# Kernel tuning notes

Hardware: AMD Instinct MI355X
Metric: run time of the kernel (lower is better)

Reference implementation:

```python
import jax, jax.numpy as jnp
import numpy as np

B, S, E, NUM_CLASSES = 4, 4096, 256, 16

def setup_inputs() -> dict:
    key = jax.random.key(0)
    ks = jax.random.split(key, 10)
    std = E ** -0.5
    return {
        "x":  jax.random.normal(ks[0], (B, S, E), dtype=jnp.float32),
        "wq": jax.random.normal(ks[1], (E, E), dtype=jnp.float32) * std,
        "bq": jnp.zeros((E,), dtype=jnp.float32),
        "wk": jax.random.normal(ks[2], (E, E), dtype=jnp.float32) * std,
        "bk": jnp.zeros((E,), dtype=jnp.float32),
        "wv": jax.random.normal(ks[3], (E, E), dtype=jnp.float32) * std,
        "bv": jnp.zeros((E,), dtype=jnp.float32),
        "wo": jax.random.normal(ks[4], (NUM_CLASSES, E), dtype=jnp.float32) * std,
        "bo": jnp.zeros((NUM_CLASSES,), dtype=jnp.float32),
    }

def reference(x, wq, bq, wk, bk, wv, bv, wo, bo):
    embed_dim = wq.shape[0]
    scaling = embed_dim ** -0.5  # float(embed_dim) ** (-0.5)
    # torch Linear: y = x @ W.T + b
    Q = jnp.einsum('bse,oe->bso', x, wq) + bq
    K = jnp.einsum('bse,oe->bso', x, wk) + bk
    V = jnp.einsum('bse,oe->bso', x, wv) + bv
    # scores: [B, S, S]
    scores = jnp.einsum('bqe,bke->bqk', Q, K) * scaling
    # original code has `/ (embed_dim ^ 0.5)`; intended math is / sqrt(embed_dim)
    attn = jax.nn.softmax(scores, axis=-1) * scaling
    attn_out = jnp.einsum('bqk,bke->bqe', attn, V)
    return jnp.einsum('bqe,oe->bqo', attn_out, wo) + bo
```

## Files before the change

kernel.cpp:

```cpp
#include <hip/hip_runtime.h>
#include <hip/hip_bf16.h>


#define S_ 4096
#define E_ 256
#define B_ 4
#define NC_ 16
#define BS_ (B_ * S_)
#define NS_ 4

typedef __attribute__((ext_vector_type(8))) short bf16x8;
typedef __attribute__((ext_vector_type(4))) float f32x4;

__device__ __forceinline__ unsigned short bf16_rtne(float f) {
    unsigned int u = __float_as_uint(f);
    return (unsigned short)((u + 0x7FFFu + ((u >> 16) & 1u)) >> 16);
}
__device__ __forceinline__ bf16x8 pack8(f32x4 a, f32x4 b) {
    bf16x8 r;
#pragma unroll
    for (int i = 0; i < 4; i++) r[i] = (short)bf16_rtne(a[i]);
#pragma unroll
    for (int i = 0; i < 4; i++) r[4 + i] = (short)bf16_rtne(b[i]);
    return r;
}
__device__ __forceinline__ void gl_lds16(const void* g, void* lds) {
    __builtin_amdgcn_global_load_lds(
        (const __attribute__((address_space(1))) unsigned int*)g,
        (__attribute__((address_space(3))) unsigned int*)lds, 16, 0, 0);
}

__global__ __launch_bounds__(256) void qkv_gemm(
    const float* __restrict__ x, const float* __restrict__ wq,
    const float* __restrict__ wk, const float* __restrict__ wv,
    const float* __restrict__ bq, const float* __restrict__ bk,
    const float* __restrict__ bv, short* __restrict__ Qb,
    short* __restrict__ Kb, short* __restrict__ Vtc) {
    __shared__ bf16x8 xt2[512];
    __shared__ bf16x8 wt2[2048];
    __shared__ short epi[16896];

    int t = threadIdx.x;
    int sel = blockIdx.x, m0 = blockIdx.y * 64;
    int lane = t & 63, wid = t >> 6, quad = lane >> 4, idx = lane & 15;

    const float* w = (sel == 0) ? wq : (sel == 1) ? wk : wv;
    const float* bias = (sel == 0) ? bq : (sel == 1) ? bk : bv;

    const float* xsrc = x + (size_t)(m0 + (t >> 2)) * E_ + (t & 3) * 8;

    f32x4 zf = {0.f, 0.f, 0.f, 0.f};
    f32x4 acc[16];
#pragma unroll
    for (int i = 0; i < 16; i++) acc[i] = zf;

    f32x4 xa0 = *(const f32x4*)xsrc;
    f32x4 xa1 = *(const f32x4*)(xsrc + 4);
    f32x4 wa[4][2];
#pragma unroll
    for (int i = 0; i < 4; i++) {
        int p = i * 256 + t;
        const float* ws = w + (size_t)(p >> 2) * E_ + (p & 3) * 8;
        wa[i][0] = *(const f32x4*)ws;
        wa[i][1] = *(const f32x4*)(ws + 4);
    }

    for (int kci = 0; kci < 8; kci++) {
        int par = kci & 1;
        xt2[par * 256 + t] = pack8(xa0, xa1);
#pragma unroll
        for (int i = 0; i < 4; i++) wt2[par * 1024 + i * 256 + t] = pack8(wa[i][0], wa[i][1]);
        if (kci < 7) {
            int kc = (kci + 1) * 32;
            xa0 = *(const f32x4*)(xsrc + kc);
            xa1 = *(const f32x4*)(xsrc + kc + 4);
#pragma unroll
            for (int i = 0; i < 4; i++) {
                int p = i * 256 + t;
                const float* ws = w + (size_t)(p >> 2) * E_ + (p & 3) * 8 + kc;
                wa[i][0] = *(const f32x4*)ws;
                wa[i][1] = *(const f32x4*)(ws + 4);
            }
        }
        __syncthreads();
        bf16x8 af = xt2[par * 256 + (wid * 16 + idx) * 4 + quad];
#pragma unroll
        for (int ct = 0; ct < 16; ct++)
            acc[ct] = __builtin_amdgcn_mfma_f32_16x16x32_bf16(
                af, wt2[par * 1024 + (ct * 16 + idx) * 4 + quad], acc[ct], 0, 0, 0);
    }
    __syncthreads();

    int qr = quad * 4;
    if (sel == 2) {
#pragma unroll
        for (int ct = 0; ct < 16; ct++) {
            int e = ct * 16 + idx;
            float bb = bias[e];
#pragma unroll
            for (int r = 0; r < 4; r++) {
                int mr = wid * 16 + qr + r;
                int ckg = mr >> 5, sin = mr & 31;
                int sp = ((sin & 15) << 1) | (sin >> 4);
                int pos = (sp >> 3) ^ ((e >> 1) & 3);
                epi[ckg * 8192 + e * 32 + pos * 8 + (sp & 7)] =
                    (short)bf16_rtne(acc[ct][r] + bb);
            }
        }
        __syncthreads();
        size_t base = ((size_t)((m0 >> 12) * 128 + ((m0 & (S_ - 1)) >> 5))) * 8192;
#pragma unroll
        for (int j = 0; j < 8; j++) {
            int unit = j * 256 + t;
            *(bf16x8*)(Vtc + base + (size_t)unit * 8) = *(const bf16x8*)&epi[unit * 8];
        }
    } else {
        float alpha = (sel == 0) ? 0.0625f : 1.0f;
#pragma unroll
        for (int ct = 0; ct < 16; ct++) {
            int n = ct * 16 + idx;
            float bb = bias[n];
#pragma unroll
            for (int r = 0; r < 4; r++) {
                int row = wid * 16 + qr + r;
                int col = (sel == 1) ? ((((n >> 3) ^ (row & 7)) << 3) | (n & 7)) : n;
                epi[row * 264 + col] = (short)bf16_rtne((acc[ct][r] + bb) * alpha);
            }
        }
        __syncthreads();
        short* out = (sel == 0) ? Qb : Kb;
#pragma unroll
        for (int j = 0; j < 8; j++) {
            int g = j * 256 + t;
            int row = g >> 5, seg = g & 31;
            *(bf16x8*)(out + (size_t)(m0 + row) * E_ + seg * 8) =
                *(const bf16x8*)&epi[row * 264 + seg * 8];
        }
    }
}

__global__ __launch_bounds__(256, 2) void flash_attn(
    const short* __restrict__ Qb, const short* __restrict__ Kb,
    const short* __restrict__ Vtc, short* __restrict__ Opart,
    float* __restrict__ lpart) {
    __shared__ __align__(16) short lds[36864];

    int t = threadIdx.x;
    int b = blockIdx.z, slice = blockIdx.y, q0 = blockIdx.x * 128;
    int key0 = slice * (S_ / NS_);
    const int nchunk = (S_ / NS_) / 32;
    int lane = t & 63, wv = t >> 6, quad = lane >> 4, idx = lane & 15;

    bf16x8 qf[2][8];
#pragma unroll
    for (int u = 0; u < 2; u++) {
        const short* qrow = Qb + (size_t)(b * S_ + q0 + u * 64 + wv * 16 + idx) * E_ + quad * 8;
#pragma unroll
        for (int c = 0; c < 8; c++) qf[u][c] = *(const bf16x8*)(qrow + c * 32);
    }

    f32x4 zf = {0.f, 0.f, 0.f, 0.f};
    f32x4 oacc[2][16];
#pragma unroll
    for (int u = 0; u < 2; u++)
#pragma unroll
        for (int i = 0; i < 16; i++) oacc[u][i] = zf;
    float ls[2][4] = {{0, 0, 0, 0}, {0, 0, 0, 0}};

    const short* kg = Kb + (size_t)(b * S_ + key0) * E_ + lane * 8;
    const short* vg = Vtc + ((size_t)(b * 128 + (key0 >> 5))) * 8192 + lane * 8;
    short* psw = lds + 32768 + wv * 1024;
    unsigned int* pswu = (unsigned int*)psw;
    int vsw = (quad ^ ((idx >> 1) & 3)) << 3;

#pragma unroll
    for (int j = 0; j < 4; j++) gl_lds16(kg + (wv * 4 + j) * 512, &lds[(wv * 4 + j) * 512]);
#pragma unroll
    for (int j = 0; j < 4; j++) gl_lds16(vg + (wv * 4 + j) * 512, &lds[16384 + (wv * 4 + j) * 512]);
#pragma unroll
    for (int j = 0; j < 4; j++) gl_lds16(kg + 8192 + (wv * 4 + j) * 512, &lds[8192 + (wv * 4 + j) * 512]);
    __syncthreads();

    {
        f32x4 s[4] = {zf, zf, zf, zf};
#pragma unroll
        for (int c = 0; c < 8; c++) {
            int p = (((c * 4 + quad) ^ (idx & 7)) << 3);
            bf16x8 k0 = *(const bf16x8*)&lds[idx * 256 + p];
            bf16x8 k1 = *(const bf16x8*)&lds[(16 + idx) * 256 + p];
            s[0] = __builtin_amdgcn_mfma_f32_16x16x32_bf16(qf[0][c], k0, s[0], 0, 0, 0);
            s[1] = __builtin_amdgcn_mfma_f32_16x16x32_bf16(qf[0][c], k1, s[1], 0, 0, 0);
            s[2] = __builtin_amdgcn_mfma_f32_16x16x32_bf16(qf[1][c], k0, s[2], 0, 0, 0);
            s[3] = __builtin_amdgcn_mfma_f32_16x16x32_bf16(qf[1][c], k1, s[3], 0, 0, 0);
        }
#pragma unroll
        for (int r = 0; r < 4; r++) {
            float a0 = __expf(s[0][r]), a1 = __expf(s[1][r]);
            float c0 = __expf(s[2][r]), c1 = __expf(s[3][r]);
            ls[0][r] += a0 + a1;
            ls[1][r] += c0 + c1;
            pswu[(quad * 4 + r) * 16 + idx] =
                (unsigned int)bf16_rtne(a0) | ((unsigned int)bf16_rtne(a1) << 16);
            pswu[256 + (quad * 4 + r) * 16 + idx] =
                (unsigned int)bf16_rtne(c0) | ((unsigned int)bf16_rtne(c1) << 16);
        }
    }

    for (int ck = 0; ck < nchunk - 1; ck++) {
        __syncthreads();
        if (ck + 2 < nchunk) {
            const short* ks = kg + (size_t)(ck + 2) * 8192;
            short* kd = lds + (ck & 1) * 8192;
#pragma unroll
            for (int j = 0; j < 4; j++) gl_lds16(ks + (wv * 4 + j) * 512, &kd[(wv * 4 + j) * 512]);
        }
        {
            const short* vs = vg + (size_t)(ck + 1) * 8192;
            short* vd = lds + 16384 + ((ck + 1) & 1) * 8192;
#pragma unroll
            for (int j = 0; j < 4; j++) gl_lds16(vs + (wv * 4 + j) * 512, &vd[(wv * 4 + j) * 512]);
        }
        const short* kc = lds + ((ck + 1) & 1) * 8192;
        f32x4 s[4] = {zf, zf, zf, zf};
#pragma unroll
        for (int c = 0; c < 8; c++) {
            int p = (((c * 4 + quad) ^ (idx & 7)) << 3);
            bf16x8 k0 = *(const bf16x8*)&kc[idx * 256 + p];
            bf16x8 k1 = *(const bf16x8*)&kc[(16 + idx) * 256 + p];
            s[0] = __builtin_amdgcn_mfma_f32_16x16x32_bf16(qf[0][c], k0, s[0], 0, 0, 0);
            s[1] = __builtin_amdgcn_mfma_f32_16x16x32_bf16(qf[0][c], k1, s[1], 0, 0, 0);
            s[2] = __builtin_amdgcn_mfma_f32_16x16x32_bf16(qf[1][c], k0, s[2], 0, 0, 0);
            s[3] = __builtin_amdgcn_mfma_f32_16x16x32_bf16(qf[1][c], k1, s[3], 0, 0, 0);
        }
        bf16x8 af0 = *(const bf16x8*)&psw[idx * 32 + quad * 8];
        bf16x8 af1 = *(const bf16x8*)&psw[512 + idx * 32 + quad * 8];
#pragma unroll
        for (int r = 0; r < 4; r++) {
            float a0 = __expf(s[0][r]), a1 = __expf(s[1][r]);
            float c0 = __expf(s[2][r]), c1 = __expf(s[3][r]);
            ls[0][r] += a0 + a1;
            ls[1][r] += c0 + c1;
            pswu[(quad * 4 + r) * 16 + idx] =
                (unsigned int)bf16_rtne(a0) | ((unsigned int)bf16_rtne(a1) << 16);
            pswu[256 + (quad * 4 + r) * 16 + idx] =
                (unsigned int)bf16_rtne(c0) | ((unsigned int)bf16_rtne(c1) << 16);
        }
        const short* vc = lds + 16384 + (ck & 1) * 8192;
#pragma unroll
        for (int ct = 0; ct < 16; ct++) {
            bf16x8 v = *(const bf16x8*)&vc[(ct * 16 + idx) * 32 + vsw];
            oacc[0][ct] = __builtin_amdgcn_mfma_f32_16x16x32_bf16(af0, v, oacc[0][ct], 0, 0, 0);
            oacc[1][ct] = __builtin_amdgcn_mfma_f32_16x16x32_bf16(af1, v, oacc[1][ct], 0, 0, 0);
        }
    }
    __syncthreads();
    {
        bf16x8 af0 = *(const bf16x8*)&psw[idx * 32 + quad * 8];
        bf16x8 af1 = *(const bf16x8*)&psw[512 + idx * 32 + quad * 8];
        const short* vc = lds + 16384 + ((nchunk - 1) & 1) * 8192;
#pragma unroll
        for (int ct = 0; ct < 16; ct++) {
            bf16x8 v = *(const bf16x8*)&vc[(ct * 16 + idx) * 32 + vsw];
            oacc[0][ct] = __builtin_amdgcn_mfma_f32_16x16x32_bf16(af0, v, oacc[0][ct], 0, 0, 0);
            oacc[1][ct] = __builtin_amdgcn_mfma_f32_16x16x32_bf16(af1, v, oacc[1][ct], 0, 0, 0);
        }
    }
    __syncthreads();

#pragma unroll
    for (int u = 0; u < 2; u++)
#pragma unroll
        for (int r = 0; r < 4; r++) {
            float v = ls[u][r];
            v += __shfl_xor(v, 1);
            v += __shfl_xor(v, 2);
            v += __shfl_xor(v, 4);
            v += __shfl_xor(v, 8);
            if (idx == 0)
                lpart[(size_t)slice * BS_ + b * S_ + q0 + u * 64 + wv * 16 + quad * 4 + r] = v;
        }

    short* scr = lds + wv * 8192;
#pragma unroll
    for (int u = 0; u < 2; u++)
#pragma unroll
        for (int ct = 0; ct < 16; ct++) {
            int e = ct * 16 + idx;
#pragma unroll
            for (int r = 0; r < 4; r++) {
                int lr = quad * 4 + r;
                scr[u * 4096 + lr * 256 + ((((e >> 3) ^ (lr & 7)) << 3) | (e & 7))] =
                    (short)bf16_rtne(oacc[u][ct][r]);
            }
        }
#pragma unroll
    for (int u = 0; u < 2; u++) {
        size_t obase = ((size_t)slice * BS_ + (size_t)b * S_ + q0 + u * 64 + wv * 16) * E_;
#pragma unroll
        for (int j = 0; j < 8; j++) {
            int unit = j * 64 + lane;
            *(bf16x8*)(Opart + obase + (size_t)unit * 8) =
                *(const bf16x8*)&scr[u * 4096 + unit * 8];
        }
    }
}

__global__ __launch_bounds__(256) void proj_out(
    const short* __restrict__ Opart, const float* __restrict__ lpart,
    const float* __restrict__ wo, const float* __restrict__ bo,
    float* __restrict__ out) {
    __shared__ __align__(16) short at2[2][16384];
    int t = threadIdx.x;
    int m0 = blockIdx.x * 64;
    int lane = t & 63, wv = t >> 6, quad = lane >> 4, idx = lane & 15;

    bf16x8 bw[8];
#pragma unroll
    for (int c = 0; c < 8; c++) {
        const float* ws = wo + idx * E_ + c * 32 + quad * 8;
        f32x4 w0 = *(const f32x4*)ws;
        f32x4 w1 = *(const f32x4*)(ws + 4);
        bw[c] = pack8(w0, w1);
    }

#pragma unroll
    for (int j = 0; j < 8; j++)
        gl_lds16(Opart + (size_t)m0 * E_ + (wv * 8 + j) * 512 + lane * 8,
                 &at2[0][(wv * 8 + j) * 512]);

    f32x4 acc = {0.f, 0.f, 0.f, 0.f};
    for (int ns = 0; ns < NS_; ns++) {
        __syncthreads();
        if (ns + 1 < NS_) {
            const short* src = Opart + ((size_t)(ns + 1) * BS_ + m0) * E_ + lane * 8;
#pragma unroll
            for (int j = 0; j < 8; j++)
                gl_lds16(src + (wv * 8 + j) * 512, &at2[(ns + 1) & 1][(wv * 8 + j) * 512]);
        }
        const short* a = at2[ns & 1];
#pragma unroll
        for (int c = 0; c < 8; c++) {
            bf16x8 af = *(const bf16x8*)&a[(wv * 16 + idx) * 256 +
                                           ((((c * 4 + quad) ^ (idx & 7)) << 3))];
            acc = __builtin_amdgcn_mfma_f32_16x16x32_bf16(af, bw[c], acc, 0, 0, 0);
        }
    }
#pragma unroll
    for (int r = 0; r < 4; r++) {
        int m = m0 + wv * 16 + quad * 4 + r;
        float ltot = 0.f;
#pragma unroll
        for (int ns = 0; ns < NS_; ns++) ltot += lpart[(size_t)ns * BS_ + m];
        out[(size_t)m * NC_ + idx] = acc[r] * (0.0625f / ltot) + bo[idx];
    }
}

extern "C" void kernel_launch(void* const* d_in, const int* in_sizes, int n_in,
                              void* d_out, int out_size, void* d_ws, size_t ws_size,
                              hipStream_t stream) {
    const float* x  = (const float*)d_in[0];
    const float* wq = (const float*)d_in[1];
    const float* bq = (const float*)d_in[2];
    const float* wk = (const float*)d_in[3];
    const float* bk = (const float*)d_in[4];
    const float* wv = (const float*)d_in[5];
    const float* bv = (const float*)d_in[6];
    const float* wo = (const float*)d_in[7];
    const float* bo = (const float*)d_in[8];
    float* out = (float*)d_out;

    const size_t NEL = (size_t)BS_ * E_;
    short* Qb = (short*)d_ws;
    short* Kb = Qb + NEL;
    short* Vtc = Kb + NEL;
    short* Opart = Vtc + NEL;
    float* lpart = (float*)(Opart + (size_t)NS_ * NEL);

    qkv_gemm<<<dim3(3, BS_ / 64), 256, 0, stream>>>(x, wq, wk, wv, bq, bk, bv, Qb, Kb, Vtc);
    flash_attn<<<dim3(S_ / 128, NS_, B_), 256, 0, stream>>>(Qb, Kb, Vtc, Opart, lpart);
    proj_out<<<BS_ / 64, 256, 0, stream>>>(Opart, lpart, wo, bo, out);
}
```

Baseline: 182.5 us.

## Fuse output projection into flash attention epilogue with atomic split-K reduction

```diff
diff --git a/kernel.cpp b/kernel.cpp
--- a/kernel.cpp
+++ b/kernel.cpp
@@ -141,8 +141,8 @@
 
 __global__ __launch_bounds__(256, 2) void flash_attn(
     const short* __restrict__ Qb, const short* __restrict__ Kb,
-    const short* __restrict__ Vtc, short* __restrict__ Opart,
-    float* __restrict__ lpart) {
+    const short* __restrict__ Vtc, const float* __restrict__ wo,
+    float* __restrict__ acc, float* __restrict__ ltot) {
     __shared__ __align__(16) short lds[36864];
 
     int t = threadIdx.x;
@@ -157,6 +157,14 @@
         const short* qrow = Qb + (size_t)(b * S_ + q0 + u * 64 + wv * 16 + idx) * E_ + quad * 8;
 #pragma unroll
         for (int c = 0; c < 8; c++) qf[u][c] = *(const bf16x8*)(qrow + c * 32);
+    }
+    bf16x8 bw[8];
+#pragma unroll
+    for (int c = 0; c < 8; c++) {
+        const float* ws = wo + idx * E_ + c * 32 + quad * 8;
+        f32x4 w0 = *(const f32x4*)ws;
+        f32x4 w1 = *(const f32x4*)(ws + 4);
+        bw[c] = pack8(w0, w1);
     }
 
     f32x4 zf = {0.f, 0.f, 0.f, 0.f};
@@ -277,7 +285,7 @@
             v += __shfl_xor(v, 4);
             v += __shfl_xor(v, 8);
             if (idx == 0)
-                lpart[(size_t)slice * BS_ + b * S_ + q0 + u * 64 + wv * 16 + quad * 4 + r] = v;
+                atomicAdd(&ltot[(size_t)b * S_ + q0 + u * 64 + wv * 16 + quad * 4 + r], v);
         }
 
     short* scr = lds + wv * 8192;
@@ -293,66 +301,34 @@
                     (short)bf16_rtne(oacc[u][ct][r]);
             }
         }
-#pragma unroll
-    for (int u = 0; u < 2; u++) {
-        size_t obase = ((size_t)slice * BS_ + (size_t)b * S_ + q0 + u * 64 + wv * 16) * E_;
-#pragma unroll
-        for (int j = 0; j < 8; j++) {
-            int unit = j * 64 + lane;
-            *(bf16x8*)(Opart + obase + (size_t)unit * 8) =
-                *(const bf16x8*)&scr[u * 4096 + unit * 8];
-        }
-    }
-}
-
-__global__ __launch_bounds__(256) void proj_out(
-    const short* __restrict__ Opart, const float* __restrict__ lpart,
-    const float* __restrict__ wo, const float* __restrict__ bo,
-    float* __restrict__ out) {
-    __shared__ __align__(16) short at2[2][16384];
-    int t = threadIdx.x;
-    int m0 = blockIdx.x * 64;
-    int lane = t & 63, wv = t >> 6, quad = lane >> 4, idx = lane & 15;
-
-    bf16x8 bw[8];
-#pragma unroll
-    for (int c = 0; c < 8; c++) {
-        const float* ws = wo + idx * E_ + c * 32 + quad * 8;
-        f32x4 w0 = *(const f32x4*)ws;
-        f32x4 w1 = *(const f32x4*)(ws + 4);
-        bw[c] = pack8(w0, w1);
-    }
-
-#pragma unroll
-    for (int j = 0; j < 8; j++)
-        gl_lds16(Opart + (size_t)m0 * E_ + (wv * 8 + j) * 512 + lane * 8,
-                 &at2[0][(wv * 8 + j) * 512]);
-
-    f32x4 acc = {0.f, 0.f, 0.f, 0.f};
-    for (int ns = 0; ns < NS_; ns++) {
-        __syncthreads();
-        if (ns + 1 < NS_) {
-            const short* src = Opart + ((size_t)(ns + 1) * BS_ + m0) * E_ + lane * 8;
-#pragma unroll
-            for (int j = 0; j < 8; j++)
-                gl_lds16(src + (wv * 8 + j) * 512, &at2[(ns + 1) & 1][(wv * 8 + j) * 512]);
-        }
-        const short* a = at2[ns & 1];
+    f32x4 pacc[2] = {zf, zf};
+#pragma unroll
+    for (int u = 0; u < 2; u++)
 #pragma unroll
         for (int c = 0; c < 8; c++) {
-            bf16x8 af = *(const bf16x8*)&a[(wv * 16 + idx) * 256 +
-                                           ((((c * 4 + quad) ^ (idx & 7)) << 3))];
-            acc = __builtin_amdgcn_mfma_f32_16x16x32_bf16(af, bw[c], acc, 0, 0, 0);
-        }
-    }
-#pragma unroll
-    for (int r = 0; r < 4; r++) {
-        int m = m0 + wv * 16 + quad * 4 + r;
-        float ltot = 0.f;
-#pragma unroll
-        for (int ns = 0; ns < NS_; ns++) ltot += lpart[(size_t)ns * BS_ + m];
-        out[(size_t)m * NC_ + idx] = acc[r] * (0.0625f / ltot) + bo[idx];
-    }
+            bf16x8 afp = *(const bf16x8*)&scr[u * 4096 + idx * 256 +
+                                              ((((c * 4 + quad) ^ (idx & 7)) << 3))];
+            pacc[u] = __builtin_amdgcn_mfma_f32_16x16x32_bf16(afp, bw[c], pacc[u], 0, 0, 0);
+        }
+#pragma unroll
+    for (int u = 0; u < 2; u++)
+#pragma unroll
+        for (int r = 0; r < 4; r++) {
+            size_t m = (size_t)b * S_ + q0 + u * 64 + wv * 16 + quad * 4 + r;
+            atomicAdd(&acc[m * NC_ + idx], pacc[u][r]);
+        }
+}
+
+__global__ __launch_bounds__(256) void finalize(
+    const float* __restrict__ acc, const float* __restrict__ ltot,
+    const float* __restrict__ bo, float* __restrict__ out) {
+    int g = blockIdx.x * 256 + threadIdx.x;
+    f32x4 a = ((const f32x4*)acc)[g];
+    int m = g >> 2;
+    float s = 0.0625f / ltot[m];
+    f32x4 b4 = ((const f32x4*)bo)[g & 3];
+    f32x4 r = {a[0] * s + b4[0], a[1] * s + b4[1], a[2] * s + b4[2], a[3] * s + b4[3]};
+    ((f32x4*)out)[g] = r;
 }
 
 extern "C" void kernel_launch(void* const* d_in, const int* in_sizes, int n_in,
@@ -373,10 +349,11 @@
     short* Qb = (short*)d_ws;
     short* Kb = Qb + NEL;
     short* Vtc = Kb + NEL;
-    short* Opart = Vtc + NEL;
-    float* lpart = (float*)(Opart + (size_t)NS_ * NEL);
-
+    float* acc = (float*)(Vtc + NEL);
+    float* ltot = acc + (size_t)BS_ * NC_;
+
+    hipMemsetAsync(acc, 0, ((size_t)BS_ * NC_ + BS_) * sizeof(float), stream);
     qkv_gemm<<<dim3(3, BS_ / 64), 256, 0, stream>>>(x, wq, wk, wv, bq, bk, bv, Qb, Kb, Vtc);
-    flash_attn<<<dim3(S_ / 128, NS_, B_), 256, 0, stream>>>(Qb, Kb, Vtc, Opart, lpart);
-    proj_out<<<BS_ / 64, 256, 0, stream>>>(Opart, lpart, wo, bo, out);
-}
+    flash_attn<<<dim3(S_ / 128, NS_, B_), 256, 0, stream>>>(Qb, Kb, Vtc, wo, acc, ltot);
+    finalize<<<(BS_ * NC_ / 4) / 256, 256, 0, stream>>>(acc, ltot, bo, out);
+}
```

Measured after the change: 181.9 us. About the same (-0.3%).
